# Kernel tuning notes

Measured on AMD Instinct MI355X. Metric: run time of the kernel, lower is better.

Reference implementation:

```python
import jax, jax.numpy as jnp
import numpy as np

DIM = 2048
HEADS = 16
DIM_HEAD = 128
DIM_INNER = HEADS * DIM_HEAD  # 2048
EPS = 1.1920929e-07  # torch RMSNorm default eps = finfo(float32).eps


def setup_inputs() -> dict:
    key = jax.random.key(0)
    k_tok, k_q, k_kv, k_o = jax.random.split(key, 4)
    tokens = jax.random.normal(k_tok, (4, 2048, DIM), dtype=jnp.float32)
    # Linear weights stored as [in, out]; torch init ~ U(-1/sqrt(in), 1/sqrt(in)), use scaled normal
    s = 0.02
    w_q = jax.random.normal(k_q, (DIM, DIM_INNER), dtype=jnp.float32) * s
    w_kv = jax.random.normal(k_kv, (DIM, 2 * DIM_INNER), dtype=jnp.float32) * s
    w_out = jax.random.normal(k_o, (DIM_INNER, DIM), dtype=jnp.float32) * s
    norm_weight = jnp.ones((DIM,), dtype=jnp.float32)
    return {"tokens": tokens, "norm_weight": norm_weight, "w_q": w_q, "w_kv": w_kv, "w_out": w_out}


def _rmsnorm(x, weight):
    var = jnp.mean(jnp.square(x), axis=-1, keepdims=True)
    return x * jax.lax.rsqrt(var + EPS) * weight


def reference(tokens, norm_weight, w_q, w_kv, w_out):
    b, n, _ = tokens.shape
    x = _rmsnorm(tokens, norm_weight)
    q = x @ w_q                       # [b, n, h*d]
    kv = x @ w_kv                     # [b, n, 2*h*d]
    k, v = jnp.split(kv, 2, axis=-1)

    def split_heads(t):
        return t.reshape(b, n, HEADS, DIM_HEAD).transpose(0, 2, 1, 3)  # b h n d

    q, k, v = map(split_heads, (q, k, v))
    q = q * (DIM_HEAD ** -0.5)
    sim = jnp.einsum('bhid,bhjd->bhij', q, k)
    attn = jax.nn.softmax(sim, axis=-1)
    out = jnp.einsum('bhij,bhjd->bhid', attn, v)
    out = out.transpose(0, 2, 1, 3).reshape(b, n, DIM_INNER)
    return out @ w_out
```

## Files before the change

### kernel.cpp

```cpp
#include <hip/hip_runtime.h>
#include <hip/hip_bf16.h>
#include <stdint.h>

#define SEQ   2048
#define DIM   2048
#define HEADS 16
#define DHEAD 128
#define BATCH 4
#define MROWS (BATCH*SEQ)

typedef short bf16x8 __attribute__((ext_vector_type(8)));
typedef float f32x4  __attribute__((ext_vector_type(4)));
typedef float f32x16 __attribute__((ext_vector_type(16)));
typedef unsigned short u16x8 __attribute__((ext_vector_type(8)));
typedef unsigned int u32x4 __attribute__((ext_vector_type(4)));

__device__ __forceinline__ short f2bf(float f){
  union { float fv; unsigned u; } x; x.fv = f;
  unsigned r = x.u + 0x7fffu + ((x.u >> 16) & 1u);
  return (short)(r >> 16);
}

__device__ __forceinline__ unsigned cvtpk(float lo, float hi){
  unsigned r; asm("v_cvt_pk_bf16_f32 %0, %1, %2" : "=v"(r) : "v"(lo), "v"(hi)); return r;
}

__device__ __forceinline__ float exp2a(float x){
#if __has_builtin(__builtin_amdgcn_exp2f)
  return __builtin_amdgcn_exp2f(x);
#else
  return exp2f(x);
#endif
}

__device__ __forceinline__ void gl_lds16(const void* g, void* l){
  __builtin_amdgcn_global_load_lds((const __attribute__((address_space(1))) void*)g,
                                   (__attribute__((address_space(3))) void*)l, 16, 0, 0);
}

__device__ __forceinline__ void ofence(){
  asm volatile("" ::: "memory");
  __builtin_amdgcn_sched_barrier(0);
}

__global__ __launch_bounds__(256) void rmsnorm_cast_k(const float* __restrict__ tok,
                                                      const float* __restrict__ w,
                                                      short* __restrict__ x){
  const int row = blockIdx.x;
  const float4* r4 = (const float4*)(tok + (size_t)row * DIM);
  float4 a = r4[threadIdx.x * 2];
  float4 b = r4[threadIdx.x * 2 + 1];
  float ss = a.x*a.x + a.y*a.y + a.z*a.z + a.w*a.w
           + b.x*b.x + b.y*b.y + b.z*b.z + b.w*b.w;
  #pragma unroll
  for (int m = 1; m < 64; m <<= 1) ss += __shfl_xor(ss, m, 64);
  __shared__ float red[4];
  if ((threadIdx.x & 63) == 0) red[threadIdx.x >> 6] = ss;
  __syncthreads();
  float tot = red[0] + red[1] + red[2] + red[3];
  float rs = rsqrtf(tot * (1.0f / DIM) + 1.1920929e-07f);
  const float4* w4 = (const float4*)w;
  float4 wa = w4[threadIdx.x * 2];
  float4 wb = w4[threadIdx.x * 2 + 1];
  u16x8 o;
  o[0] = (unsigned short)f2bf(a.x * rs * wa.x);
  o[1] = (unsigned short)f2bf(a.y * rs * wa.y);
  o[2] = (unsigned short)f2bf(a.z * rs * wa.z);
  o[3] = (unsigned short)f2bf(a.w * rs * wa.w);
  o[4] = (unsigned short)f2bf(b.x * rs * wb.x);
  o[5] = (unsigned short)f2bf(b.y * rs * wb.y);
  o[6] = (unsigned short)f2bf(b.z * rs * wb.z);
  o[7] = (unsigned short)f2bf(b.w * rs * wb.w);
  *(u16x8*)(x + (size_t)row * DIM + threadIdx.x * 8) = o;
}

__global__ __launch_bounds__(256) void wtrans_k(const float* __restrict__ w,
                                                short* __restrict__ wt,
                                                int K, int N){
  __shared__ float tile[64][65];
  const int r0 = blockIdx.y * 64;
  const int c0 = blockIdx.x * 64;
  const int t = threadIdx.x;
  #pragma unroll
  for (int i = 0; i < 16; i++){
    int e = i * 256 + t; int r = e >> 6, c = e & 63;
    tile[r][c] = w[(size_t)(r0 + r) * N + c0 + c];
  }
  __syncthreads();
  #pragma unroll
  for (int i = 0; i < 16; i++){
    int e = i * 256 + t; int c = e >> 6, r = e & 63;
    wt[(size_t)(c0 + c) * K + r0 + r] = f2bf(tile[r][c]);
  }
}

__global__ __launch_bounds__(256) void vtrans_k(const short* __restrict__ kv,
                                                short* __restrict__ vt){
  __shared__ short tile[64][65];
  const int n0 = blockIdx.x * 64;
  const int d0 = blockIdx.y * 64;
  const int bh = blockIdx.z;
  const int b = bh >> 4, h = bh & 15;
  const int t = threadIdx.x;
  #pragma unroll
  for (int i = 0; i < 16; i++){
    int e = i * 256 + t; int r = e >> 6, c = e & 63;
    tile[r][c] = kv[(size_t)(b * SEQ + n0 + r) * 4096 + 2048 + h * DHEAD + d0 + c];
  }
  __syncthreads();
  #pragma unroll
  for (int i = 0; i < 16; i++){
    int e = i * 256 + t; int c = e >> 6, r = e & 63;
    vt[(size_t)(bh * DHEAD + d0 + c) * SEQ + n0 + r] = tile[r][c];
  }
}

__device__ __forceinline__ void storeC(float* C, size_t idx, float v){ C[idx] = v; }
__device__ __forceinline__ void storeC(short* C, size_t idx, float v){ C[idx] = f2bf(v); }

template<typename OutT>
__global__ __launch_bounds__(512, 2) void gemm256_k(const short* __restrict__ A,
                                                    const short* __restrict__ Bt,
                                                    OutT* __restrict__ C,
                                                    int M, int N, int K, int lgntn){
  __shared__ __align__(16) short As[4][256 * 32];
  __shared__ __align__(16) short Bs[4][256 * 32];
  const int nwg = gridDim.x;
  const int bid = blockIdx.x;
  const int o = (bid & 7) * (nwg >> 3) + (bid >> 3);
  const int bm = o >> lgntn, bn = o & ((1 << lgntn) - 1);
  const int m0 = bm << 8, n0 = bn << 8;
  const int tid = threadIdx.x, lane = tid & 63, wid = tid >> 6;
  const int l31 = lane & 31, hi = lane >> 5;
  const int wr = wid >> 2, wc = wid & 3;
  const int NT = K >> 5;

  f32x16 acc[4][2] = {};

  auto stage = [&](int t){
    const int slot = t & 3;
    const size_t kbase = (size_t)t << 5;
    #pragma unroll
    for (int i = 0; i < 2; i++){
      int c = i * 512 + tid;
      int row = c >> 2;
      int j = (c & 3) ^ ((row >> 1) & 3);
      gl_lds16(A + (size_t)(m0 + row) * K + kbase + j * 8,
               &As[slot][(i * 512 + wid * 64) * 8]);
    }
    #pragma unroll
    for (int i = 0; i < 2; i++){
      int c = i * 512 + tid;
      int row = c >> 2;
      int j = (c & 3) ^ ((row >> 1) & 3);
      gl_lds16(Bt + (size_t)(n0 + row) * K + kbase + j * 8,
               &Bs[slot][(i * 512 + wid * 64) * 8]);
    }
  };

  auto compute = [&](int t){
    const short* Ab = As[t & 3];
    const short* Bb = Bs[t & 3];
    bf16x8 af[4][2], bfv[2][2];
    #pragma unroll
    for (int mb = 0; mb < 4; mb++){
      int row = wr * 128 + mb * 32 + l31;
      #pragma unroll
      for (int ks = 0; ks < 2; ks++){
        int ch = (ks * 2 + hi) ^ ((row >> 1) & 3);
        af[mb][ks] = *(const bf16x8*)&Ab[row * 32 + ch * 8];
      }
    }
    #pragma unroll
    for (int nb = 0; nb < 2; nb++){
      int row = wc * 64 + nb * 32 + l31;
      #pragma unroll
      for (int ks = 0; ks < 2; ks++){
        int ch = (ks * 2 + hi) ^ ((row >> 1) & 3);
        bfv[nb][ks] = *(const bf16x8*)&Bb[row * 32 + ch * 8];
      }
    }
    __builtin_amdgcn_s_setprio(1);
    #pragma unroll
    for (int mb = 0; mb < 4; mb++)
      #pragma unroll
      for (int nb = 0; nb < 2; nb++)
        #pragma unroll
        for (int ks = 0; ks < 2; ks++)
          acc[mb][nb] = __builtin_amdgcn_mfma_f32_32x32x16_bf16(af[mb][ks], bfv[nb][ks],
                                                                acc[mb][nb], 0, 0, 0);
    __builtin_amdgcn_s_setprio(0);
  };

  stage(0); ofence();
  stage(1); ofence();
  stage(2); ofence();
  asm volatile("s_waitcnt vmcnt(8)" ::: "memory");
  __builtin_amdgcn_s_barrier();

  for (int t = 0; t < NT; t++){
    if (t + 3 < NT){ stage(t + 3); ofence(); }
    compute(t);
    if (t + 1 < NT){
      if (t + 3 < NT)      asm volatile("s_waitcnt vmcnt(8)" ::: "memory");
      else if (t + 2 < NT) asm volatile("s_waitcnt vmcnt(4)" ::: "memory");
      else                 asm volatile("s_waitcnt vmcnt(0)" ::: "memory");
      __builtin_amdgcn_s_barrier();
    }
  }

  #pragma unroll
  for (int mb = 0; mb < 4; mb++)
    #pragma unroll
    for (int nb = 0; nb < 2; nb++)
      #pragma unroll
      for (int reg = 0; reg < 16; reg++){
        int r = (reg & 3) + 8 * (reg >> 2) + 4 * hi;
        int row = m0 + wr * 128 + mb * 32 + r;
        int col = n0 + wc * 64 + nb * 32 + l31;
        storeC(C, (size_t)row * N + col, acc[mb][nb][reg]);
      }
}

__global__ __launch_bounds__(256) void attn_k(const short* __restrict__ q,
                                              const short* __restrict__ kv,
                                              const short* __restrict__ vt,
                                              short* __restrict__ out){
  __shared__ __align__(16) short Ks[2][64 * 128];
  __shared__ __align__(16) short Vts[128 * 64];
  const int qt = blockIdx.x, bh = blockIdx.y;
  const int b = bh >> 4, h = bh & 15;
  const int tid = threadIdx.x, lane = tid & 63, wid = tid >> 6;
  const int l31 = lane & 31, hi = lane >> 5;
  const int qrow0 = qt * 128 + wid * 32;
  const float c2 = 0.08838834764831845f * 1.4426950408889634f;
  const int NT = SEQ / 64;

  bf16x8 qf[8];
  {
    const short* qp = q + (size_t)(b * SEQ + qrow0 + l31) * DIM + h * DHEAD + hi * 8;
    #pragma unroll
    for (int s = 0; s < 8; s++) qf[s] = *(const bf16x8*)(qp + s * 16);
  }
  ofence();

  f32x16 acc[4] = {};
  float m2 = -3e38f, l_s = 0.f;

  auto stage_K = [&](int kt, int bs){
    #pragma unroll
    for (int i = 0; i < 4; i++){
      int cb = (i * 4 + wid) * 64;
      int c  = cb + lane;
      int kr = c >> 4, kj = (c & 15) ^ (kr & 7);
      gl_lds16(kv + (size_t)(b * SEQ + kt * 64 + kr) * 4096 + h * DHEAD + kj * 8,
               &Ks[bs][cb * 8]);
    }
  };
  auto stage_V = [&](int kt){
    #pragma unroll
    for (int i = 0; i < 4; i++){
      int cb = (i * 4 + wid) * 64;
      int c  = cb + lane;
      int vr = c >> 3, vj = (c & 7) ^ (vr & 7);
      gl_lds16(vt + (size_t)(bh * DHEAD + vr) * SEQ + kt * 64 + vj * 8,
               &Vts[cb * 8]);
    }
  };

  stage_K(0, 0); ofence();

  for (int kt = 0; kt < NT; kt++){
    const int cur = kt & 1;
    stage_V(kt); ofence();
    if (kt + 1 < NT){ stage_K(kt + 1, cur ^ 1); ofence(); }
    if (kt == 0){
      asm volatile("s_waitcnt vmcnt(8)" ::: "memory");
      __builtin_amdgcn_s_barrier();
    }

    const short* Kb = Ks[cur];

    f32x16 t0 = {0,0,0,0,0,0,0,0,0,0,0,0,0,0,0,0};
    f32x16 t1 = t0;
    {
      const int r0 = l31, r1 = l31 + 32;
      #pragma unroll
      for (int s = 0; s < 8; s++){
        bf16x8 k0 = *(const bf16x8*)&Kb[r0 * 128 + (((2 * s + hi) ^ (r0 & 7)) * 8)];
        bf16x8 k1 = *(const bf16x8*)&Kb[r1 * 128 + (((2 * s + hi) ^ (r1 & 7)) * 8)];
        t0 = __builtin_amdgcn_mfma_f32_32x32x16_bf16(k0, qf[s], t0, 0, 0, 0);
        t1 = __builtin_amdgcn_mfma_f32_32x32x16_bf16(k1, qf[s], t1, 0, 0, 0);
      }
    }

    float mr[8];
    #pragma unroll
    for (int i = 0; i < 8; i++)
      mr[i] = fmaxf(fmaxf(t0[i], t0[i + 8]), fmaxf(t1[i], t1[i + 8]));
    #pragma unroll
    for (int s = 4; s > 0; s >>= 1)
      #pragma unroll
      for (int i = 0; i < s; i++) mr[i] = fmaxf(mr[i], mr[i + s]);
    float mxr = fmaxf(mr[0], __shfl_xor(mr[0], 32));
    float mx2 = mxr * c2;
    if (!__all(mx2 <= m2 + 11.5f)){
      float m2n = fmaxf(m2, mx2);
      float al = exp2a(m2 - m2n);
      m2 = m2n;
      l_s *= al;
      #pragma unroll
      for (int reg = 0; reg < 16; reg++){
        float ar = __shfl(al, (reg & 3) + 8 * (reg >> 2) + 4 * hi);
        #pragma unroll
        for (int dt = 0; dt < 4; dt++) acc[dt][reg] *= ar;
      }
    }

    float ps0 = 0.f, ps1 = 0.f, ps2 = 0.f, ps3 = 0.f;
    unsigned w[16];
    #pragma unroll
    for (int pr = 0; pr < 8; pr++){
      float pa_ = exp2a(fmaf(t0[2 * pr], c2, -m2));
      float pb_ = exp2a(fmaf(t0[2 * pr + 1], c2, -m2));
      ps0 += pa_; ps1 += pb_;
      w[pr] = cvtpk(pa_, pb_);
    }
    #pragma unroll
    for (int pr = 0; pr < 8; pr++){
      float pa_ = exp2a(fmaf(t1[2 * pr], c2, -m2));
      float pb_ = exp2a(fmaf(t1[2 * pr + 1], c2, -m2));
      ps2 += pa_; ps3 += pb_;
      w[8 + pr] = cvtpk(pa_, pb_);
    }
    float ps = (ps0 + ps1) + (ps2 + ps3);
    ps += __shfl_xor(ps, 32);
    l_s += ps;

    if (kt + 1 < NT) asm volatile("s_waitcnt vmcnt(4)" ::: "memory");
    else             asm volatile("s_waitcnt vmcnt(0)" ::: "memory");
    __builtin_amdgcn_s_barrier();

    #pragma unroll
    for (int fp = 0; fp < 4; fp++){
      unsigned A0 = w[fp * 4 + 0], A1 = w[fp * 4 + 1];
      unsigned B0 = w[fp * 4 + 2], B1 = w[fp * 4 + 3];
      unsigned xA0 = __shfl_xor((int)A0, 32), xA1 = __shfl_xor((int)A1, 32);
      unsigned xB0 = __shfl_xor((int)B0, 32), xB1 = __shfl_xor((int)B1, 32);
      u32x4 fw;
      fw[0] = hi ? xB0 : A0;
      fw[1] = hi ? xB1 : A1;
      fw[2] = hi ? B0 : xA0;
      fw[3] = hi ? B1 : xA1;
      union { u32x4 u; bf16x8 v; } pc; pc.u = fw;
      #pragma unroll
      for (int dt = 0; dt < 4; dt++){
        int vr = dt * 32 + l31;
        bf16x8 vb = *(const bf16x8*)&Vts[vr * 64 + (((2 * fp + hi) ^ (vr & 7)) * 8)];
        acc[dt] = __builtin_amdgcn_mfma_f32_32x32x16_bf16(pc.v, vb, acc[dt], 0, 0, 0);
      }
    }

    asm volatile("s_waitcnt vmcnt(0) lgkmcnt(0)" ::: "memory");
    __builtin_amdgcn_s_barrier();
  }

  float inv = 1.0f / l_s;
  #pragma unroll
  for (int reg = 0; reg < 16; reg++){
    int cr = (reg & 3) + 8 * (reg >> 2) + 4 * hi;
    float li = __shfl(inv, cr);
    int row = qrow0 + cr;
    #pragma unroll
    for (int dt = 0; dt < 4; dt++)
      out[(size_t)(b * SEQ + row) * DIM + h * DHEAD + dt * 32 + l31] = f2bf(acc[dt][reg] * li);
  }
}

extern "C" void kernel_launch(void* const* d_in, const int* in_sizes, int n_in,
                              void* d_out, int out_size, void* d_ws, size_t ws_size,
                              hipStream_t stream) {
  (void)in_sizes; (void)n_in; (void)out_size; (void)ws_size;
  const float* tokens = (const float*)d_in[0];
  const float* normw  = (const float*)d_in[1];
  const float* wq     = (const float*)d_in[2];
  const float* wkv    = (const float*)d_in[3];
  const float* wout   = (const float*)d_in[4];
  float* outp = (float*)d_out;
  char* ws = (char*)d_ws;

  short* x     = (short*)(ws + 0);
  short* wqt   = (short*)(ws + 33554432);
  short* wkvt  = (short*)(ws + 41943040);
  short* woutt = (short*)(ws + 58720256);
  short* qb    = (short*)(ws + 67108864);
  short* kvb   = (short*)(ws + 100663296);
  short* vtb   = (short*)(ws + 167772160);

  rmsnorm_cast_k<<<dim3(MROWS), dim3(256), 0, stream>>>(tokens, normw, x);
  wtrans_k<<<dim3(2048/64, 2048/64), dim3(256), 0, stream>>>(wq,   wqt,   2048, 2048);
  wtrans_k<<<dim3(4096/64, 2048/64), dim3(256), 0, stream>>>(wkv,  wkvt,  2048, 4096);
  wtrans_k<<<dim3(2048/64, 2048/64), dim3(256), 0, stream>>>(wout, woutt, 2048, 2048);
  gemm256_k<short><<<dim3((MROWS/256)*(2048/256)), dim3(512), 0, stream>>>(x, wqt,  qb,  MROWS, 2048, 2048, 3);
  gemm256_k<short><<<dim3((MROWS/256)*(4096/256)), dim3(512), 0, stream>>>(x, wkvt, kvb, MROWS, 4096, 2048, 4);
  vtrans_k<<<dim3(SEQ/64, DHEAD/64, BATCH*HEADS), dim3(256), 0, stream>>>(kvb, vtb);
  attn_k<<<dim3(SEQ/128, BATCH*HEADS), dim3(256), 0, stream>>>(qb, kvb, vtb, qb);
  gemm256_k<float><<<dim3((MROWS/256)*(2048/256)), dim3(512), 0, stream>>>(qb, woutt, outp, MROWS, 2048, 2048, 3);
}
```

Measured before the change: 649.3 us.

## Load K/V fragments directly from global memory and remap blocks across XCDs

The attention kernel drops LDS staging, double buffering and barriers, and each wave now loads its K and V^T MFMA fragments straight from global memory, processing 32-key sub-tiles. The grid is flattened to 1D and block ids are permuted so that blocks sharing a batch-head land on the same XCD, which should improve L2 reuse of K/V. The aim is to remove LDS traffic and barrier stalls, at the cost of four waves each re-reading the same K/V from cache instead of sharing one LDS copy, plus exposed global load latency with no explicit prefetch.

```diff
diff --git a/kernel.cpp b/kernel.cpp
--- a/kernel.cpp
+++ b/kernel.cpp
@@ -226,9 +226,9 @@
                                               const short* __restrict__ kv,
                                               const short* __restrict__ vt,
                                               short* __restrict__ out){
-  __shared__ __align__(16) short Ks[2][64 * 128];
-  __shared__ __align__(16) short Vts[128 * 64];
-  const int qt = blockIdx.x, bh = blockIdx.y;
+  const int bid = blockIdx.x, nb = gridDim.x;
+  const int o = (bid & 7) * (nb >> 3) + (bid >> 3);
+  const int qt = o & 15, bh = o >> 4;
   const int b = bh >> 4, h = bh & 15;
   const int tid = threadIdx.x, lane = tid & 63, wid = tid >> 6;
   const int l31 = lane & 31, hi = lane >> 5;
@@ -242,127 +242,87 @@
     #pragma unroll
     for (int s = 0; s < 8; s++) qf[s] = *(const bf16x8*)(qp + s * 16);
   }
-  ofence();
+
+  const short* kb0 = kv + (size_t)(b * SEQ + l31) * 4096 + h * DHEAD + hi * 8;
+  const short* vb0 = vt + ((size_t)bh * DHEAD + l31) * SEQ + hi * 8;
 
   f32x16 acc[4] = {};
   float m2 = -3e38f, l_s = 0.f;
 
-  auto stage_K = [&](int kt, int bs){
-    #pragma unroll
-    for (int i = 0; i < 4; i++){
-      int cb = (i * 4 + wid) * 64;
-      int c  = cb + lane;
-      int kr = c >> 4, kj = (c & 15) ^ (kr & 7);
-      gl_lds16(kv + (size_t)(b * SEQ + kt * 64 + kr) * 4096 + h * DHEAD + kj * 8,
-               &Ks[bs][cb * 8]);
-    }
-  };
-  auto stage_V = [&](int kt){
-    #pragma unroll
-    for (int i = 0; i < 4; i++){
-      int cb = (i * 4 + wid) * 64;
-      int c  = cb + lane;
-      int vr = c >> 3, vj = (c & 7) ^ (vr & 7);
-      gl_lds16(vt + (size_t)(bh * DHEAD + vr) * SEQ + kt * 64 + vj * 8,
-               &Vts[cb * 8]);
-    }
-  };
-
-  stage_K(0, 0); ofence();
-
   for (int kt = 0; kt < NT; kt++){
-    const int cur = kt & 1;
-    stage_V(kt); ofence();
-    if (kt + 1 < NT){ stage_K(kt + 1, cur ^ 1); ofence(); }
-    if (kt == 0){
-      asm volatile("s_waitcnt vmcnt(8)" ::: "memory");
-      __builtin_amdgcn_s_barrier();
-    }
-
-    const short* Kb = Ks[cur];
-
-    f32x16 t0 = {0,0,0,0,0,0,0,0,0,0,0,0,0,0,0,0};
-    f32x16 t1 = t0;
-    {
-      const int r0 = l31, r1 = l31 + 32;
-      #pragma unroll
-      for (int s = 0; s < 8; s++){
-        bf16x8 k0 = *(const bf16x8*)&Kb[r0 * 128 + (((2 * s + hi) ^ (r0 & 7)) * 8)];
-        bf16x8 k1 = *(const bf16x8*)&Kb[r1 * 128 + (((2 * s + hi) ^ (r1 & 7)) * 8)];
-        t0 = __builtin_amdgcn_mfma_f32_32x32x16_bf16(k0, qf[s], t0, 0, 0, 0);
-        t1 = __builtin_amdgcn_mfma_f32_32x32x16_bf16(k1, qf[s], t1, 0, 0, 0);
-      }
-    }
-
-    float mr[8];
-    #pragma unroll
-    for (int i = 0; i < 8; i++)
-      mr[i] = fmaxf(fmaxf(t0[i], t0[i + 8]), fmaxf(t1[i], t1[i + 8]));
-    #pragma unroll
-    for (int s = 4; s > 0; s >>= 1)
-      #pragma unroll
-      for (int i = 0; i < s; i++) mr[i] = fmaxf(mr[i], mr[i + s]);
-    float mxr = fmaxf(mr[0], __shfl_xor(mr[0], 32));
-    float mx2 = mxr * c2;
-    if (!__all(mx2 <= m2 + 11.5f)){
-      float m2n = fmaxf(m2, mx2);
-      float al = exp2a(m2 - m2n);
-      m2 = m2n;
-      l_s *= al;
-      #pragma unroll
-      for (int reg = 0; reg < 16; reg++){
-        float ar = __shfl(al, (reg & 3) + 8 * (reg >> 2) + 4 * hi);
-        #pragma unroll
-        for (int dt = 0; dt < 4; dt++) acc[dt][reg] *= ar;
-      }
-    }
-
-    float ps0 = 0.f, ps1 = 0.f, ps2 = 0.f, ps3 = 0.f;
-    unsigned w[16];
-    #pragma unroll
-    for (int pr = 0; pr < 8; pr++){
-      float pa_ = exp2a(fmaf(t0[2 * pr], c2, -m2));
-      float pb_ = exp2a(fmaf(t0[2 * pr + 1], c2, -m2));
-      ps0 += pa_; ps1 += pb_;
-      w[pr] = cvtpk(pa_, pb_);
-    }
-    #pragma unroll
-    for (int pr = 0; pr < 8; pr++){
-      float pa_ = exp2a(fmaf(t1[2 * pr], c2, -m2));
-      float pb_ = exp2a(fmaf(t1[2 * pr + 1], c2, -m2));
-      ps2 += pa_; ps3 += pb_;
-      w[8 + pr] = cvtpk(pa_, pb_);
-    }
-    float ps = (ps0 + ps1) + (ps2 + ps3);
-    ps += __shfl_xor(ps, 32);
-    l_s += ps;
-
-    if (kt + 1 < NT) asm volatile("s_waitcnt vmcnt(4)" ::: "memory");
-    else             asm volatile("s_waitcnt vmcnt(0)" ::: "memory");
-    __builtin_amdgcn_s_barrier();
-
-    #pragma unroll
-    for (int fp = 0; fp < 4; fp++){
-      unsigned A0 = w[fp * 4 + 0], A1 = w[fp * 4 + 1];
-      unsigned B0 = w[fp * 4 + 2], B1 = w[fp * 4 + 3];
-      unsigned xA0 = __shfl_xor((int)A0, 32), xA1 = __shfl_xor((int)A1, 32);
-      unsigned xB0 = __shfl_xor((int)B0, 32), xB1 = __shfl_xor((int)B1, 32);
-      u32x4 fw;
-      fw[0] = hi ? xB0 : A0;
-      fw[1] = hi ? xB1 : A1;
-      fw[2] = hi ? B0 : xA0;
-      fw[3] = hi ? B1 : xA1;
-      union { u32x4 u; bf16x8 v; } pc; pc.u = fw;
-      #pragma unroll
-      for (int dt = 0; dt < 4; dt++){
-        int vr = dt * 32 + l31;
-        bf16x8 vb = *(const bf16x8*)&Vts[vr * 64 + (((2 * fp + hi) ^ (vr & 7)) * 8)];
-        acc[dt] = __builtin_amdgcn_mfma_f32_32x32x16_bf16(pc.v, vb, acc[dt], 0, 0, 0);
-      }
-    }
-
-    asm volatile("s_waitcnt vmcnt(0) lgkmcnt(0)" ::: "memory");
-    __builtin_amdgcn_s_barrier();
+    #pragma unroll
+    for (int ksub = 0; ksub < 2; ksub++){
+      const int key0 = kt * 64 + ksub * 32;
+
+      const short* kr = kb0 + (size_t)key0 * 4096;
+      bf16x8 kf[8];
+      #pragma unroll
+      for (int s = 0; s < 8; s++) kf[s] = *(const bf16x8*)(kr + s * 16);
+
+      f32x16 t = {0,0,0,0,0,0,0,0,0,0,0,0,0,0,0,0};
+      #pragma unroll
+      for (int s = 0; s < 8; s++)
+        t = __builtin_amdgcn_mfma_f32_32x32x16_bf16(kf[s], qf[s], t, 0, 0, 0);
+
+      bf16x8 vf[2][4];
+      #pragma unroll
+      for (int fpl = 0; fpl < 2; fpl++)
+        #pragma unroll
+        for (int dt = 0; dt < 4; dt++)
+          vf[fpl][dt] = *(const bf16x8*)(vb0 + (size_t)(dt * 32) * SEQ + key0 + fpl * 16);
+
+      float mr[8];
+      #pragma unroll
+      for (int i = 0; i < 8; i++) mr[i] = fmaxf(t[i], t[i + 8]);
+      #pragma unroll
+      for (int s = 4; s > 0; s >>= 1)
+        #pragma unroll
+        for (int i = 0; i < s; i++) mr[i] = fmaxf(mr[i], mr[i + s]);
+      float mxr = fmaxf(mr[0], __shfl_xor(mr[0], 32));
+      float mx2 = mxr * c2;
+      if (!__all(mx2 <= m2 + 11.5f)){
+        float m2n = fmaxf(m2, mx2);
+        float al = exp2a(m2 - m2n);
+        m2 = m2n;
+        l_s *= al;
+        #pragma unroll
+        for (int reg = 0; reg < 16; reg++){
+          float ar = __shfl(al, (reg & 3) + 8 * (reg >> 2) + 4 * hi);
+          #pragma unroll
+          for (int dt = 0; dt < 4; dt++) acc[dt][reg] *= ar;
+        }
+      }
+
+      float p0 = 0.f, p1 = 0.f;
+      unsigned w[8];
+      #pragma unroll
+      for (int pr = 0; pr < 8; pr++){
+        float pa_ = exp2a(fmaf(t[2 * pr], c2, -m2));
+        float pb_ = exp2a(fmaf(t[2 * pr + 1], c2, -m2));
+        p0 += pa_; p1 += pb_;
+        w[pr] = cvtpk(pa_, pb_);
+      }
+      float ps = p0 + p1;
+      ps += __shfl_xor(ps, 32);
+      l_s += ps;
+
+      #pragma unroll
+      for (int fpl = 0; fpl < 2; fpl++){
+        unsigned A0 = w[fpl * 4 + 0], A1 = w[fpl * 4 + 1];
+        unsigned B0 = w[fpl * 4 + 2], B1 = w[fpl * 4 + 3];
+        unsigned xA0 = __shfl_xor((int)A0, 32), xA1 = __shfl_xor((int)A1, 32);
+        unsigned xB0 = __shfl_xor((int)B0, 32), xB1 = __shfl_xor((int)B1, 32);
+        u32x4 fw;
+        fw[0] = hi ? xB0 : A0;
+        fw[1] = hi ? xB1 : A1;
+        fw[2] = hi ? B0 : xA0;
+        fw[3] = hi ? B1 : xA1;
+        union { u32x4 u; bf16x8 v; } pc; pc.u = fw;
+        #pragma unroll
+        for (int dt = 0; dt < 4; dt++)
+          acc[dt] = __builtin_amdgcn_mfma_f32_32x32x16_bf16(pc.v, vf[fpl][dt], acc[dt], 0, 0, 0);
+      }
+    }
   }
 
   float inv = 1.0f / l_s;
@@ -404,6 +364,6 @@
   gemm256_k<short><<<dim3((MROWS/256)*(2048/256)), dim3(512), 0, stream>>>(x, wqt,  qb,  MROWS, 2048, 2048, 3);
   gemm256_k<short><<<dim3((MROWS/256)*(4096/256)), dim3(512), 0, stream>>>(x, wkvt, kvb, MROWS, 4096, 2048, 4);
   vtrans_k<<<dim3(SEQ/64, DHEAD/64, BATCH*HEADS), dim3(256), 0, stream>>>(kvb, vtb);
-  attn_k<<<dim3(SEQ/128, BATCH*HEADS), dim3(256), 0, stream>>>(qb, kvb, vtb, qb);
+  attn_k<<<dim3(SEQ/128 * BATCH*HEADS), dim3(256), 0, stream>>>(qb, kvb, vtb, qb);
   gemm256_k<float><<<dim3((MROWS/256)*(2048/256)), dim3(512), 0, stream>>>(qb, woutt, outp, MROWS, 2048, 2048, 3);
 }
```

New measurement: 841.3 us. 29.6% more time.
